# Kernel tuning notes

Measured on AMD Instinct MI355X. Metric: run time of the kernel, lower is better.

Reference implementation:

```python
import jax, jax.numpy as jnp
import numpy as np

N_USERS = 50000
N_ITEMS = 50000
N_NODES = N_USERS + N_ITEMS
N_EDGES = 1600000
D_IN = 128
D_OUT = 128


def setup_inputs() -> dict:
    key = jax.random.key(0)
    k1, k2, k3, k4, k5, k6 = jax.random.split(key, 6)
    u_f = jax.random.normal(k1, (N_USERS, D_IN), dtype=jnp.float32)
    v_f = jax.random.normal(k2, (N_ITEMS, D_IN), dtype=jnp.float32)
    adj_rows = jax.random.randint(k3, (N_EDGES,), 0, N_NODES, dtype=jnp.int32)
    adj_cols = jax.random.randint(k4, (N_EDGES,), 0, N_NODES, dtype=jnp.int32)
    adj_vals = jax.random.uniform(k5, (N_EDGES,), dtype=jnp.float32)
    # xavier_uniform init for weight [in_feats, out_feats]
    bound = float(np.sqrt(6.0 / (D_IN + D_OUT)))
    weight = jax.random.uniform(k6, (D_IN, D_OUT), dtype=jnp.float32,
                                minval=-bound, maxval=bound)
    return {"u_f": u_f, "v_f": v_f, "adj_rows": adj_rows,
            "adj_cols": adj_cols, "adj_vals": adj_vals, "weight": weight}


def reference(u_f, v_f, adj_rows, adj_cols, adj_vals, weight):
    # node_f = cat([u_f, v_f]) @ W          -- dense transform
    node_f = jnp.concatenate([u_f, v_f], axis=0)          # [N, D_in]
    node_f = node_f @ weight                               # [N, D_out]
    # sparse adjacency matmul: out[r] = sum_e vals[e] * node_f[cols[e]]
    msgs = adj_vals[:, None] * node_f[adj_cols]            # [E, D_out]
    out = jax.ops.segment_sum(msgs, adj_rows, num_segments=N_NODES)
    # activation (relu)
    return jax.nn.relu(out)
```

## Files before the change

kernel.cpp:

```cpp
#include <hip/hip_runtime.h>
#include <hip/hip_bf16.h>
#include <hip/hip_fp16.h>

#define N_USERS 50000
#define N_NODES 100000
#define N_EDGES 1600000
#define DIM 128
#define CAP 64

#define RPB 128
#define NBINS ((N_NODES + RPB - 1) / RPB)
#define BINCAP 4096
#define EPB 8192
#define FILL_BLOCKS ((N_EDGES + EPB - 1) / EPB)
#define GEMM_BLOCKS 1024
#define FUSED_GRID (GEMM_BLOCKS + FILL_BLOCKS)
#define WFRAG_ELEMS (32 * 64 * 8)

typedef __attribute__((ext_vector_type(8))) _Float16 half8;
typedef __attribute__((ext_vector_type(4))) _Float16 half4;
typedef __attribute__((ext_vector_type(4))) float f32x4;

__global__ void prep_kernel(const float* __restrict__ W,
                            _Float16* __restrict__ wfrag_g,
                            int* __restrict__ gcount) {
    if (blockIdx.x == 64) {
        for (int b = threadIdx.x; b < NBINS; b += 256) gcount[b] = 0;
        return;
    }
    const int f   = blockIdx.x * 256 + threadIdx.x;
    const int ts  = f >> 9;
    const int rem = f & 511;
    const int ln  = rem >> 3;
    const int j   = rem & 7;
    const int t   = ts >> 2;
    const int s   = ts & 3;
    const int krow = s * 32 + (ln >> 4) * 8 + j;
    const int col  = t * 16 + (ln & 15);
    wfrag_g[f] = (_Float16)W[krow * DIM + col];
}

__device__ __forceinline__ void gemm_main(
        const float* __restrict__ u_f, const float* __restrict__ v_f,
        _Float16* __restrict__ node_f, const _Float16* wfrag,
        int blockId, int nBlocks) {
    const int tid  = threadIdx.x;
    const int lane = tid & 63;
    const int wave = tid >> 6;
    const int m    = lane & 15;
    const int quad = lane >> 4;
    const int n_wtiles = N_NODES / 16;

    for (int wt = blockId * 4 + wave; wt < n_wtiles; wt += nBlocks * 4) {
        const int row = wt * 16 + m;
        const float* src = (row < N_USERS) ? u_f + (size_t)row * DIM
                                           : v_f + (size_t)(row - N_USERS) * DIM;
        f32x4 acc[8];
        #pragma unroll
        for (int t = 0; t < 8; ++t) acc[t] = (f32x4){0.f, 0.f, 0.f, 0.f};

        #pragma unroll
        for (int s = 0; s < 4; ++s) {
            const float* ap = src + s * 32 + quad * 8;
            const float4 a0 = *(const float4*)ap;
            const float4 a1 = *(const float4*)(ap + 4);
            half8 af;
            af[0] = (_Float16)a0.x; af[1] = (_Float16)a0.y;
            af[2] = (_Float16)a0.z; af[3] = (_Float16)a0.w;
            af[4] = (_Float16)a1.x; af[5] = (_Float16)a1.y;
            af[6] = (_Float16)a1.z; af[7] = (_Float16)a1.w;
            #pragma unroll
            for (int t = 0; t < 8; ++t) {
                const half8 wf = *(const half8*)&wfrag[((t * 4 + s) * 64 + lane) * 8];
                acc[t] = __builtin_amdgcn_mfma_f32_16x16x32_f16(af, wf, acc[t], 0, 0, 0);
            }
        }

        const int base = wt * 16;
        #pragma unroll
        for (int t = 0; t < 8; ++t) {
            #pragma unroll
            for (int r = 0; r < 4; ++r) {
                const int orow = base + quad * 4 + r;
                node_f[(size_t)orow * DIM + t * 16 + m] = (_Float16)acc[t][r];
            }
        }
    }
}

__global__ __launch_bounds__(256) void fused_gemm_fill_kernel(
        const float* __restrict__ u_f, const float* __restrict__ v_f,
        const _Float16* __restrict__ wfrag_g, _Float16* __restrict__ node_f,
        const int* __restrict__ rows, const int* __restrict__ cols,
        const float* __restrict__ vals,
        int* __restrict__ gcount, long long* __restrict__ bin_data) {
    __shared__ union {
        _Float16 wfrag[WFRAG_ELEMS];
        struct { int hist[NBINS]; int base_[NBINS]; } a;
    } sh;

    if (blockIdx.x >= FILL_BLOCKS) {
        const int4* src = (const int4*)wfrag_g;
        int4* dst = (int4*)sh.wfrag;
        #pragma unroll
        for (int i = 0; i < WFRAG_ELEMS / 8 / 256; ++i)
            dst[i * 256 + threadIdx.x] = src[i * 256 + threadIdx.x];
        __syncthreads();
        gemm_main(u_f, v_f, node_f, sh.wfrag,
                  blockIdx.x - FILL_BLOCKS, GEMM_BLOCKS);
        return;
    }

    const int bb  = blockIdx.x;
    const int tid = threadIdx.x;
    const int e0  = bb * EPB;

    for (int b = tid; b < NBINS; b += 256) sh.a.hist[b] = 0;
    __syncthreads();

    unsigned meta[EPB / 256];
    #pragma unroll
    for (int i = 0; i < EPB / 256; ++i) {
        const int e = e0 + i * 256 + tid;
        if (e < N_EDGES) {
            const int row = rows[e];
            const int bin = row >> 7;
            const int pos = atomicAdd(&sh.a.hist[bin], 1);
            meta[i] = ((unsigned)bin << 20) | ((unsigned)(row & 127) << 13)
                    | (unsigned)pos;
        } else {
            meta[i] = 0xFFFFFFFFu;
        }
    }
    __syncthreads();

    for (int b = tid; b < NBINS; b += 256) {
        const int h = sh.a.hist[b];
        sh.a.base_[b] = h ? atomicAdd(&gcount[b], h) : 0;
    }
    __syncthreads();

    #pragma unroll
    for (int i = 0; i < EPB / 256; ++i) {
        if (meta[i] == 0xFFFFFFFFu) continue;
        const int e   = e0 + i * 256 + tid;
        const int bin = meta[i] >> 20;
        const int rl  = (meta[i] >> 13) & 127;
        const int pos = meta[i] & 0x1FFF;
        const int idx = sh.a.base_[bin] + pos;
        if (idx < BINCAP) {
            const unsigned w0 = ((unsigned)rl << 17) | (unsigned)cols[e];
            const long long ent =
                ((long long)__float_as_int(vals[e]) << 32) | (long long)w0;
            bin_data[(size_t)bin * BINCAP + idx] = ent;
        }
    }
}

__global__ __launch_bounds__(256) void gemm_mfma_kernel(
        const float* __restrict__ u_f, const float* __restrict__ v_f,
        const float* __restrict__ W, _Float16* __restrict__ node_f) {
    __shared__ _Float16 wfrag[WFRAG_ELEMS];
    const int tid = threadIdx.x;
    for (int f = tid * 64, end = tid * 64 + 64; f < end; ++f) {
        const int ts   = f >> 9;
        const int rem  = f & 511;
        const int ln   = rem >> 3;
        const int j    = rem & 7;
        const int t    = ts >> 2;
        const int s    = ts & 3;
        const int krow = s * 32 + (ln >> 4) * 8 + j;
        const int col  = t * 16 + (ln & 15);
        wfrag[f] = (_Float16)W[krow * DIM + col];
    }
    __syncthreads();
    gemm_main(u_f, v_f, node_f, wfrag, blockIdx.x, gridDim.x);
}

__global__ __launch_bounds__(1024) void bin_gather_kernel(
        const _Float16* __restrict__ node_f, const int* __restrict__ gcount,
        const long long* __restrict__ bin_data, float* __restrict__ out) {
    __shared__ unsigned list[RPB][CAP];
    __shared__ int rowcnt[RPB];

    const int bin  = blockIdx.x;
    const int tid  = threadIdx.x;
    const int row0 = bin * RPB;
    const int nrows = (N_NODES - row0 < RPB) ? (N_NODES - row0) : RPB;

    if (tid < RPB) rowcnt[tid] = 0;
    __syncthreads();

    int n = gcount[bin];
    if (n > BINCAP) n = BINCAP;
    for (int k = tid; k < n; k += 1024) {
        const long long ent = bin_data[(size_t)bin * BINCAP + k];
        const unsigned w0 = (unsigned)ent;
        const float v = __int_as_float((int)(ent >> 32));
        const int rl = (int)(w0 >> 17);
        const int pos = atomicAdd(&rowcnt[rl], 1);
        if (pos < CAP) {
            const int q = (int)(v * 32767.f + 0.5f);
            list[rl][pos] = ((unsigned)q << 17) | (w0 & 0x1FFFFu);
        }
    }
    __syncthreads();

    const int wave = tid >> 6;
    const int lane = tid & 63;
    const int pid  = lane >> 4;
    const int cl   = lane & 15;

    for (int rp = 0; rp < 8; ++rp) {
        const int rl = rp * 16 + wave;
        if (rl >= nrows) break;
        const int row = row0 + rl;

        int cnt = rowcnt[rl];
        if (cnt > CAP) cnt = CAP;

        int   col = 0;
        float val = 0.f;
        if (lane < cnt) {
            const unsigned p = list[rl][lane];
            col = (int)(p & 0x1FFFFu);
            val = (float)(p >> 17) * (1.f / 32767.f);
        }

        float acc[8];
        #pragma unroll
        for (int i = 0; i < 8; ++i) acc[i] = 0.f;

        int j = 0;
        for (; j + 16 <= cnt; j += 16) {
            int c[4]; float v[4]; half8 h[4];
            #pragma unroll
            for (int q = 0; q < 4; ++q) {
                c[q] = __shfl(col, j + 4 * q + pid, 64);
                v[q] = __shfl(val, j + 4 * q + pid, 64);
            }
            #pragma unroll
            for (int q = 0; q < 4; ++q)
                h[q] = *(const half8*)&node_f[(size_t)c[q] * DIM + cl * 8];
            #pragma unroll
            for (int q = 0; q < 4; ++q) {
                #pragma unroll
                for (int i = 0; i < 8; ++i)
                    acc[i] += v[q] * (float)h[q][i];
            }
        }
        for (; j + 4 <= cnt; j += 4) {
            const int   c = __shfl(col, j + pid, 64);
            const float v = __shfl(val, j + pid, 64);
            const half8 h = *(const half8*)&node_f[(size_t)c * DIM + cl * 8];
            #pragma unroll
            for (int i = 0; i < 8; ++i)
                acc[i] += v * (float)h[i];
        }
        if (j < cnt) {
            const int rem = cnt - j;
            const int sj  = j + (pid < rem ? pid : 0);
            const int   c = __shfl(col, sj, 64);
            const float v = __shfl(val, sj, 64);
            if (pid < rem) {
                const half8 h = *(const half8*)&node_f[(size_t)c * DIM + cl * 8];
                #pragma unroll
                for (int i = 0; i < 8; ++i)
                    acc[i] += v * (float)h[i];
            }
        }

        #pragma unroll
        for (int i = 0; i < 8; ++i) {
            acc[i] += __shfl_xor(acc[i], 16, 64);
            acc[i] += __shfl_xor(acc[i], 32, 64);
        }

        if (pid == 0) {
            f32x4 r0, r1;
            #pragma unroll
            for (int i = 0; i < 4; ++i) {
                r0[i] = acc[i]     > 0.f ? acc[i]     : 0.f;
                r1[i] = acc[i + 4] > 0.f ? acc[i + 4] : 0.f;
            }
            float* dst = &out[(size_t)row * DIM + cl * 8];
            __builtin_nontemporal_store(r0, (f32x4*)dst);
            __builtin_nontemporal_store(r1, (f32x4*)(dst + 4));
        }
    }
}

__global__ void zero_out_kernel(float* __restrict__ out) {
    int i = blockIdx.x * blockDim.x + threadIdx.x;
    int idx = i * 4;
    if (idx < N_NODES * DIM) {
        float4 z = {0.f, 0.f, 0.f, 0.f};
        *(float4*)&out[idx] = z;
    }
}

__global__ void scatter_kernel(const _Float16* __restrict__ node_f,
                               const int* __restrict__ rows, const int* __restrict__ cols,
                               const float* __restrict__ vals, float* __restrict__ out) {
    int t = blockIdx.x * blockDim.x + threadIdx.x;
    int e = t >> 5;
    int part = t & 31;
    if (e >= N_EDGES) return;
    int r = rows[e], c = cols[e];
    float v = vals[e];
    const __half2 h0 = *(const __half2*)&node_f[(size_t)c * DIM + part * 4];
    const __half2 h1 = *(const __half2*)&node_f[(size_t)c * DIM + part * 4 + 2];
    const float2 f0 = __half22float2(h0);
    const float2 f1 = __half22float2(h1);
    float* dst = &out[(size_t)r * DIM + part * 4];
    unsafeAtomicAdd(dst + 0, v * f0.x);
    unsafeAtomicAdd(dst + 1, v * f0.y);
    unsafeAtomicAdd(dst + 2, v * f1.x);
    unsafeAtomicAdd(dst + 3, v * f1.y);
}

__global__ void relu_kernel(float* __restrict__ out) {
    int i = blockIdx.x * blockDim.x + threadIdx.x;
    int idx = i * 4;
    if (idx < N_NODES * DIM) {
        float4 v = *(float4*)&out[idx];
        v.x = v.x > 0.f ? v.x : 0.f;
        v.y = v.y > 0.f ? v.y : 0.f;
        v.z = v.z > 0.f ? v.z : 0.f;
        v.w = v.w > 0.f ? v.w : 0.f;
        *(float4*)&out[idx] = v;
    }
}

extern "C" void kernel_launch(void* const* d_in, const int* in_sizes, int n_in,
                              void* d_out, int out_size, void* d_ws, size_t ws_size,
                              hipStream_t stream) {
    const float* u_f  = (const float*)d_in[0];
    const float* v_f  = (const float*)d_in[1];
    const int*   rows = (const int*)d_in[2];
    const int*   cols = (const int*)d_in[3];
    const float* vals = (const float*)d_in[4];
    const float* W    = (const float*)d_in[5];
    float* out = (float*)d_out;

    char* ws = (char*)d_ws;
    const size_t nodef_bytes   = (size_t)N_NODES * DIM * 2;
    const size_t gcount_bytes  = 4096;
    const size_t bindata_bytes = (size_t)NBINS * BINCAP * 8;
    const size_t wfrag_bytes   = (size_t)WFRAG_ELEMS * 2;

    _Float16* node_f = (_Float16*)ws;
    int* gcount = (int*)(ws + nodef_bytes);
    long long* bin_data = (long long*)(ws + nodef_bytes + gcount_bytes);
    _Float16* wfrag_g = (_Float16*)(ws + nodef_bytes + gcount_bytes + bindata_bytes);

    if (ws_size >= nodef_bytes + gcount_bytes + bindata_bytes + wfrag_bytes) {
        prep_kernel<<<65, 256, 0, stream>>>(W, wfrag_g, gcount);
        fused_gemm_fill_kernel<<<FUSED_GRID, 256, 0, stream>>>(
            u_f, v_f, wfrag_g, node_f, rows, cols, vals, gcount, bin_data);
        bin_gather_kernel<<<NBINS, 1024, 0, stream>>>(
            node_f, gcount, bin_data, out);
    } else {
        gemm_mfma_kernel<<<512, 256, 0, stream>>>(u_f, v_f, W, node_f);
        zero_out_kernel<<<(N_NODES * DIM / 4 + 255) / 256, 256, 0, stream>>>(out);
        scatter_kernel<<<((size_t)N_EDGES * 32 + 255) / 256, 256, 0, stream>>>(
            node_f, rows, cols, vals, out);
        relu_kernel<<<(N_NODES * DIM / 4 + 255) / 256, 256, 0, stream>>>(out);
    }
}
```

Baseline: 232.6 us.

## Halve bin size, split columns into halves, use persistent atomic work queue

Rows per bin drop from 128 to 64, and each bin is processed as two column-half work items, so a wave covers 64 columns and eight edges run in parallel per step. Gather blocks become persistent and pull items from a global atomic counter kept in spare gcount space. The fused grid is rebalanced between GEMM and fill blocks. This aims to improve load balance and memory-level parallelism in the gather, but each bin's edge list is now read twice, and an extra reduction step plus an atomic per item are added.

```diff
diff --git a/kernel.cpp b/kernel.cpp
--- a/kernel.cpp
+++ b/kernel.cpp
@@ -8,24 +8,25 @@
 #define DIM 128
 #define CAP 64
 
-#define RPB 128
-#define NBINS ((N_NODES + RPB - 1) / RPB)
-#define BINCAP 4096
+#define RPB 64
+#define NBINS 1563
+#define BINCAP 2048
+#define NITEMS (2 * NBINS)
 #define EPB 8192
-#define FILL_BLOCKS ((N_EDGES + EPB - 1) / EPB)
-#define GEMM_BLOCKS 1024
-#define FUSED_GRID (GEMM_BLOCKS + FILL_BLOCKS)
+#define FILL_BLOCKS 196
+#define GEMM_BLOCKS 828
+#define FUSED_GRID 1024
+#define GATHER_BLOCKS 512
 #define WFRAG_ELEMS (32 * 64 * 8)
 
 typedef __attribute__((ext_vector_type(8))) _Float16 half8;
-typedef __attribute__((ext_vector_type(4))) _Float16 half4;
 typedef __attribute__((ext_vector_type(4))) float f32x4;
 
 __global__ void prep_kernel(const float* __restrict__ W,
                             _Float16* __restrict__ wfrag_g,
                             int* __restrict__ gcount) {
     if (blockIdx.x == 64) {
-        for (int b = threadIdx.x; b < NBINS; b += 256) gcount[b] = 0;
+        for (int b = threadIdx.x; b < 2048; b += 256) gcount[b] = 0;
         return;
     }
     const int f   = blockIdx.x * 256 + threadIdx.x;
@@ -124,9 +125,9 @@
         const int e = e0 + i * 256 + tid;
         if (e < N_EDGES) {
             const int row = rows[e];
-            const int bin = row >> 7;
+            const int bin = row >> 6;
             const int pos = atomicAdd(&sh.a.hist[bin], 1);
-            meta[i] = ((unsigned)bin << 20) | ((unsigned)(row & 127) << 13)
+            meta[i] = ((unsigned)bin << 20) | ((unsigned)(row & 63) << 13)
                     | (unsigned)pos;
         } else {
             meta[i] = 0xFFFFFFFFu;
@@ -179,113 +180,124 @@
 
 __global__ __launch_bounds__(1024) void bin_gather_kernel(
         const _Float16* __restrict__ node_f, const int* __restrict__ gcount,
-        const long long* __restrict__ bin_data, float* __restrict__ out) {
+        const long long* __restrict__ bin_data, float* __restrict__ out,
+        int* __restrict__ work) {
     __shared__ unsigned list[RPB][CAP];
     __shared__ int rowcnt[RPB];
-
-    const int bin  = blockIdx.x;
+    __shared__ int item_s;
+
     const int tid  = threadIdx.x;
-    const int row0 = bin * RPB;
-    const int nrows = (N_NODES - row0 < RPB) ? (N_NODES - row0) : RPB;
-
-    if (tid < RPB) rowcnt[tid] = 0;
-    __syncthreads();
-
-    int n = gcount[bin];
-    if (n > BINCAP) n = BINCAP;
-    for (int k = tid; k < n; k += 1024) {
-        const long long ent = bin_data[(size_t)bin * BINCAP + k];
-        const unsigned w0 = (unsigned)ent;
-        const float v = __int_as_float((int)(ent >> 32));
-        const int rl = (int)(w0 >> 17);
-        const int pos = atomicAdd(&rowcnt[rl], 1);
-        if (pos < CAP) {
-            const int q = (int)(v * 32767.f + 0.5f);
-            list[rl][pos] = ((unsigned)q << 17) | (w0 & 0x1FFFFu);
-        }
-    }
-    __syncthreads();
-
     const int wave = tid >> 6;
     const int lane = tid & 63;
-    const int pid  = lane >> 4;
-    const int cl   = lane & 15;
-
-    for (int rp = 0; rp < 8; ++rp) {
-        const int rl = rp * 16 + wave;
-        if (rl >= nrows) break;
-        const int row = row0 + rl;
-
-        int cnt = rowcnt[rl];
-        if (cnt > CAP) cnt = CAP;
-
-        int   col = 0;
-        float val = 0.f;
-        if (lane < cnt) {
-            const unsigned p = list[rl][lane];
-            col = (int)(p & 0x1FFFFu);
-            val = (float)(p >> 17) * (1.f / 32767.f);
-        }
-
-        float acc[8];
-        #pragma unroll
-        for (int i = 0; i < 8; ++i) acc[i] = 0.f;
-
-        int j = 0;
-        for (; j + 16 <= cnt; j += 16) {
-            int c[4]; float v[4]; half8 h[4];
+    const int pid  = lane >> 3;
+    const int cl   = lane & 7;
+
+    for (;;) {
+        __syncthreads();
+        if (tid == 0) item_s = atomicAdd(work, 1);
+        if (tid < RPB) rowcnt[tid] = 0;
+        __syncthreads();
+        const int item = item_s;
+        if (item >= NITEMS) return;
+
+        const int half = (item >= NBINS) ? 1 : 0;
+        const int bin  = item - (half ? NBINS : 0);
+        const int row0 = bin * RPB;
+        const int nrows = (N_NODES - row0 < RPB) ? (N_NODES - row0) : RPB;
+        const int cbase = half * 64 + cl * 8;
+
+        int n = gcount[bin];
+        if (n > BINCAP) n = BINCAP;
+        for (int k = tid; k < n; k += 1024) {
+            const long long ent = bin_data[(size_t)bin * BINCAP + k];
+            const unsigned w0 = (unsigned)ent;
+            const float v = __int_as_float((int)(ent >> 32));
+            const int rl = (int)(w0 >> 17);
+            const int pos = atomicAdd(&rowcnt[rl], 1);
+            if (pos < CAP) {
+                const int q = (int)(v * 32767.f + 0.5f);
+                list[rl][pos] = ((unsigned)q << 17) | (w0 & 0x1FFFFu);
+            }
+        }
+        __syncthreads();
+
+        for (int rp = 0; rp < 4; ++rp) {
+            const int rl = rp * 16 + wave;
+            if (rl >= nrows) break;
+            const int row = row0 + rl;
+
+            int cnt = rowcnt[rl];
+            if (cnt > CAP) cnt = CAP;
+
+            int   col = 0;
+            float val = 0.f;
+            if (lane < cnt) {
+                const unsigned p = list[rl][lane];
+                col = (int)(p & 0x1FFFFu);
+                val = (float)(p >> 17) * (1.f / 32767.f);
+            }
+
+            float acc[8];
             #pragma unroll
-            for (int q = 0; q < 4; ++q) {
-                c[q] = __shfl(col, j + 4 * q + pid, 64);
-                v[q] = __shfl(val, j + 4 * q + pid, 64);
-            }
-            #pragma unroll
-            for (int q = 0; q < 4; ++q)
-                h[q] = *(const half8*)&node_f[(size_t)c[q] * DIM + cl * 8];
-            #pragma unroll
-            for (int q = 0; q < 4; ++q) {
-                #pragma unroll
-                for (int i = 0; i < 8; ++i)
-                    acc[i] += v[q] * (float)h[q][i];
-            }
-        }
-        for (; j + 4 <= cnt; j += 4) {
-            const int   c = __shfl(col, j + pid, 64);
-            const float v = __shfl(val, j + pid, 64);
-            const half8 h = *(const half8*)&node_f[(size_t)c * DIM + cl * 8];
-            #pragma unroll
-            for (int i = 0; i < 8; ++i)
-                acc[i] += v * (float)h[i];
-        }
-        if (j < cnt) {
-            const int rem = cnt - j;
-            const int sj  = j + (pid < rem ? pid : 0);
-            const int   c = __shfl(col, sj, 64);
-            const float v = __shfl(val, sj, 64);
-            if (pid < rem) {
-                const half8 h = *(const half8*)&node_f[(size_t)c * DIM + cl * 8];
+            for (int i = 0; i < 8; ++i) acc[i] = 0.f;
+
+            int j = 0;
+            for (; j + 16 <= cnt; j += 16) {
+                int c[2]; float v[2]; half8 h[2];
+                #pragma unroll
+                for (int q = 0; q < 2; ++q) {
+                    c[q] = __shfl(col, j + 8 * q + pid, 64);
+                    v[q] = __shfl(val, j + 8 * q + pid, 64);
+                }
+                #pragma unroll
+                for (int q = 0; q < 2; ++q)
+                    h[q] = *(const half8*)&node_f[(size_t)c[q] * DIM + cbase];
+                #pragma unroll
+                for (int q = 0; q < 2; ++q) {
+                    #pragma unroll
+                    for (int i = 0; i < 8; ++i)
+                        acc[i] += v[q] * (float)h[q][i];
+                }
+            }
+            for (; j + 8 <= cnt; j += 8) {
+                const int   c = __shfl(col, j + pid, 64);
+                const float v = __shfl(val, j + pid, 64);
+                const half8 h = *(const half8*)&node_f[(size_t)c * DIM + cbase];
                 #pragma unroll
                 for (int i = 0; i < 8; ++i)
                     acc[i] += v * (float)h[i];
             }
-        }
-
-        #pragma unroll
-        for (int i = 0; i < 8; ++i) {
-            acc[i] += __shfl_xor(acc[i], 16, 64);
-            acc[i] += __shfl_xor(acc[i], 32, 64);
-        }
-
-        if (pid == 0) {
-            f32x4 r0, r1;
+            if (j < cnt) {
+                const int rem = cnt - j;
+                const int sj  = j + (pid < rem ? pid : 0);
+                const int   c = __shfl(col, sj, 64);
+                const float v = __shfl(val, sj, 64);
+                if (pid < rem) {
+                    const half8 h = *(const half8*)&node_f[(size_t)c * DIM + cbase];
+                    #pragma unroll
+                    for (int i = 0; i < 8; ++i)
+                        acc[i] += v * (float)h[i];
+                }
+            }
+
             #pragma unroll
-            for (int i = 0; i < 4; ++i) {
-                r0[i] = acc[i]     > 0.f ? acc[i]     : 0.f;
-                r1[i] = acc[i + 4] > 0.f ? acc[i + 4] : 0.f;
-            }
-            float* dst = &out[(size_t)row * DIM + cl * 8];
-            __builtin_nontemporal_store(r0, (f32x4*)dst);
-            __builtin_nontemporal_store(r1, (f32x4*)(dst + 4));
+            for (int i = 0; i < 8; ++i) {
+                acc[i] += __shfl_xor(acc[i], 8, 64);
+                acc[i] += __shfl_xor(acc[i], 16, 64);
+                acc[i] += __shfl_xor(acc[i], 32, 64);
+            }
+
+            if (pid == 0) {
+                f32x4 r0, r1;
+                #pragma unroll
+                for (int i = 0; i < 4; ++i) {
+                    r0[i] = acc[i]     > 0.f ? acc[i]     : 0.f;
+                    r1[i] = acc[i + 4] > 0.f ? acc[i + 4] : 0.f;
+                }
+                float* dst = &out[(size_t)row * DIM + cbase];
+                __builtin_nontemporal_store(r0, (f32x4*)dst);
+                __builtin_nontemporal_store(r1, (f32x4*)(dst + 4));
+            }
         }
     }
 }
@@ -345,7 +357,7 @@
 
     char* ws = (char*)d_ws;
     const size_t nodef_bytes   = (size_t)N_NODES * DIM * 2;
-    const size_t gcount_bytes  = 4096;
+    const size_t gcount_bytes  = 8192;
     const size_t bindata_bytes = (size_t)NBINS * BINCAP * 8;
     const size_t wfrag_bytes   = (size_t)WFRAG_ELEMS * 2;
 
@@ -358,8 +370,8 @@
         prep_kernel<<<65, 256, 0, stream>>>(W, wfrag_g, gcount);
         fused_gemm_fill_kernel<<<FUSED_GRID, 256, 0, stream>>>(
             u_f, v_f, wfrag_g, node_f, rows, cols, vals, gcount, bin_data);
-        bin_gather_kernel<<<NBINS, 1024, 0, stream>>>(
-            node_f, gcount, bin_data, out);
+        bin_gather_kernel<<<GATHER_BLOCKS, 1024, 0, stream>>>(
+            node_f, gcount, bin_data, out, gcount + 2000);
     } else {
         gemm_mfma_kernel<<<512, 256, 0, stream>>>(u_f, v_f, W, node_f);
         zero_out_kernel<<<(N_NODES * DIM / 4 + 255) / 256, 256, 0, stream>>>(out);
```

Result: slower. 251.3 us (+8.0%).

## Software-pipeline gather rows and rebalance fused GEMM/fill grid

Applied to the files above, without the earlier changes.

Restructures the per-row gather loop into issue/consume halves so that the first 16 neighbor loads of the next row are in flight while the current row is accumulated (double-buffered registers). It also changes the fused kernel grid to 828 GEMM blocks plus fill blocks totaling 1024 and adjusts gcount zeroing bound. The extra live registers for two buffered rows, together with the tighter launch bound, risk spills, and rows with more than 16 edges still fall back to serial loads.

```diff
diff --git a/kernel.cpp b/kernel.cpp
--- a/kernel.cpp
+++ b/kernel.cpp
@@ -13,19 +13,18 @@
 #define BINCAP 4096
 #define EPB 8192
 #define FILL_BLOCKS ((N_EDGES + EPB - 1) / EPB)
-#define GEMM_BLOCKS 1024
-#define FUSED_GRID (GEMM_BLOCKS + FILL_BLOCKS)
+#define GEMM_BLOCKS 828
+#define FUSED_GRID 1024
 #define WFRAG_ELEMS (32 * 64 * 8)
 
 typedef __attribute__((ext_vector_type(8))) _Float16 half8;
-typedef __attribute__((ext_vector_type(4))) _Float16 half4;
 typedef __attribute__((ext_vector_type(4))) float f32x4;
 
 __global__ void prep_kernel(const float* __restrict__ W,
                             _Float16* __restrict__ wfrag_g,
                             int* __restrict__ gcount) {
     if (blockIdx.x == 64) {
-        for (int b = threadIdx.x; b < NBINS; b += 256) gcount[b] = 0;
+        for (int b = threadIdx.x; b < 1024; b += 256) gcount[b] = 0;
         return;
     }
     const int f   = blockIdx.x * 256 + threadIdx.x;
@@ -177,7 +176,81 @@
     gemm_main(u_f, v_f, node_f, wfrag, blockIdx.x, gridDim.x);
 }
 
-__global__ __launch_bounds__(1024) void bin_gather_kernel(
+__device__ __forceinline__ void gather_issue(
+        const _Float16* __restrict__ node_f,
+        const unsigned (*list)[CAP], const int* rowcnt,
+        int nrows, int wave, int lane, int pid, int cl, int rp,
+        int& cnt, int& col, float& val, half8 h[4]) {
+    const int rl = rp * 16 + wave;
+    if (rp >= 8 || rl >= nrows) { cnt = -1; return; }
+    int c_ = rowcnt[rl]; if (c_ > CAP) c_ = CAP;
+    cnt = c_;
+    const unsigned p = (lane < c_) ? list[rl][lane] : 0u;
+    col = (int)(p & 0x1FFFFu);
+    val = (float)(p >> 17) * (1.f / 32767.f);
+    #pragma unroll
+    for (int q = 0; q < 4; ++q) {
+        const int j  = q * 4 + pid;
+        const int sj = j < c_ ? j : 0;
+        const int c  = __shfl(col, sj, 64);
+        if (j < c_)
+            h[q] = *(const half8*)&node_f[(size_t)c * DIM + cl * 8];
+    }
+}
+
+__device__ __forceinline__ void gather_consume(
+        const _Float16* __restrict__ node_f, float* __restrict__ out,
+        int row0, int wave, int pid, int cl, int rp,
+        int cnt, int col, float val, const half8 h[4]) {
+    if (cnt < 0) return;
+    const int row = row0 + rp * 16 + wave;
+
+    float acc[8];
+    #pragma unroll
+    for (int i = 0; i < 8; ++i) acc[i] = 0.f;
+
+    #pragma unroll
+    for (int q = 0; q < 4; ++q) {
+        const int j  = q * 4 + pid;
+        const int sj = j < cnt ? j : 0;
+        const float v = __shfl(val, sj, 64);
+        if (j < cnt) {
+            #pragma unroll
+            for (int i = 0; i < 8; ++i) acc[i] += v * (float)h[q][i];
+        }
+    }
+    for (int j = 16; j < cnt; j += 4) {
+        const int jj = j + pid;
+        const int sj = jj < cnt ? jj : 0;
+        const int   c = __shfl(col, sj, 64);
+        const float v = __shfl(val, sj, 64);
+        if (jj < cnt) {
+            const half8 hh = *(const half8*)&node_f[(size_t)c * DIM + cl * 8];
+            #pragma unroll
+            for (int i = 0; i < 8; ++i) acc[i] += v * (float)hh[i];
+        }
+    }
+
+    #pragma unroll
+    for (int i = 0; i < 8; ++i) {
+        acc[i] += __shfl_xor(acc[i], 16, 64);
+        acc[i] += __shfl_xor(acc[i], 32, 64);
+    }
+
+    if (pid == 0) {
+        f32x4 r0, r1;
+        #pragma unroll
+        for (int i = 0; i < 4; ++i) {
+            r0[i] = acc[i]     > 0.f ? acc[i]     : 0.f;
+            r1[i] = acc[i + 4] > 0.f ? acc[i + 4] : 0.f;
+        }
+        float* dst = &out[(size_t)row * DIM + cl * 8];
+        __builtin_nontemporal_store(r0, (f32x4*)dst);
+        __builtin_nontemporal_store(r1, (f32x4*)(dst + 4));
+    }
+}
+
+__global__ __launch_bounds__(1024, 8) void bin_gather_kernel(
         const _Float16* __restrict__ node_f, const int* __restrict__ gcount,
         const long long* __restrict__ bin_data, float* __restrict__ out) {
     __shared__ unsigned list[RPB][CAP];
@@ -211,82 +284,21 @@
     const int pid  = lane >> 4;
     const int cl   = lane & 15;
 
-    for (int rp = 0; rp < 8; ++rp) {
-        const int rl = rp * 16 + wave;
-        if (rl >= nrows) break;
-        const int row = row0 + rl;
-
-        int cnt = rowcnt[rl];
-        if (cnt > CAP) cnt = CAP;
-
-        int   col = 0;
-        float val = 0.f;
-        if (lane < cnt) {
-            const unsigned p = list[rl][lane];
-            col = (int)(p & 0x1FFFFu);
-            val = (float)(p >> 17) * (1.f / 32767.f);
-        }
-
-        float acc[8];
-        #pragma unroll
-        for (int i = 0; i < 8; ++i) acc[i] = 0.f;
-
-        int j = 0;
-        for (; j + 16 <= cnt; j += 16) {
-            int c[4]; float v[4]; half8 h[4];
-            #pragma unroll
-            for (int q = 0; q < 4; ++q) {
-                c[q] = __shfl(col, j + 4 * q + pid, 64);
-                v[q] = __shfl(val, j + 4 * q + pid, 64);
-            }
-            #pragma unroll
-            for (int q = 0; q < 4; ++q)
-                h[q] = *(const half8*)&node_f[(size_t)c[q] * DIM + cl * 8];
-            #pragma unroll
-            for (int q = 0; q < 4; ++q) {
-                #pragma unroll
-                for (int i = 0; i < 8; ++i)
-                    acc[i] += v[q] * (float)h[q][i];
-            }
-        }
-        for (; j + 4 <= cnt; j += 4) {
-            const int   c = __shfl(col, j + pid, 64);
-            const float v = __shfl(val, j + pid, 64);
-            const half8 h = *(const half8*)&node_f[(size_t)c * DIM + cl * 8];
-            #pragma unroll
-            for (int i = 0; i < 8; ++i)
-                acc[i] += v * (float)h[i];
-        }
-        if (j < cnt) {
-            const int rem = cnt - j;
-            const int sj  = j + (pid < rem ? pid : 0);
-            const int   c = __shfl(col, sj, 64);
-            const float v = __shfl(val, sj, 64);
-            if (pid < rem) {
-                const half8 h = *(const half8*)&node_f[(size_t)c * DIM + cl * 8];
-                #pragma unroll
-                for (int i = 0; i < 8; ++i)
-                    acc[i] += v * (float)h[i];
-            }
-        }
-
-        #pragma unroll
-        for (int i = 0; i < 8; ++i) {
-            acc[i] += __shfl_xor(acc[i], 16, 64);
-            acc[i] += __shfl_xor(acc[i], 32, 64);
-        }
-
-        if (pid == 0) {
-            f32x4 r0, r1;
-            #pragma unroll
-            for (int i = 0; i < 4; ++i) {
-                r0[i] = acc[i]     > 0.f ? acc[i]     : 0.f;
-                r1[i] = acc[i + 4] > 0.f ? acc[i + 4] : 0.f;
-            }
-            float* dst = &out[(size_t)row * DIM + cl * 8];
-            __builtin_nontemporal_store(r0, (f32x4*)dst);
-            __builtin_nontemporal_store(r1, (f32x4*)(dst + 4));
-        }
+    int cntA, colA; float valA; half8 hA[4];
+    int cntB, colB; float valB; half8 hB[4];
+
+    gather_issue(node_f, list, rowcnt, nrows, wave, lane, pid, cl, 0,
+                 cntA, colA, valA, hA);
+    #pragma unroll
+    for (int rp = 0; rp < 8; rp += 2) {
+        gather_issue(node_f, list, rowcnt, nrows, wave, lane, pid, cl, rp + 1,
+                     cntB, colB, valB, hB);
+        gather_consume(node_f, out, row0, wave, pid, cl, rp,
+                       cntA, colA, valA, hA);
+        gather_issue(node_f, list, rowcnt, nrows, wave, lane, pid, cl, rp + 2,
+                     cntA, colA, valA, hA);
+        gather_consume(node_f, out, row0, wave, pid, cl, rp + 1,
+                       cntB, colB, valB, hB);
     }
 }
 
```

After: 281.4 us. 21.0% more time.
